# Kernel optimization log

Hardware: AMD Instinct MI355X
Metric: run time of the kernel (lower is better)

Reference implementation:

```python
import jax, jax.numpy as jnp
import numpy as np

HIDDEN = 512
N_LAYERS = 2
SEQ = 512
BATCH = 64
H2 = HIDDEN * 2  # 1024
D_IN = H2 * (N_LAYERS + 1)  # 3072


def setup_inputs() -> dict:
    key = jax.random.key(0)
    ks = jax.random.split(key, 4)
    state = jax.random.normal(ks[0], (N_LAYERS, BATCH, H2), dtype=jnp.float32)
    encoder_output = jax.random.normal(ks[1], (SEQ, BATCH, H2), dtype=jnp.float32)
    # fc1: xavier_normal with tanh gain (5/3); fc2: kaiming_normal
    xavier_std = (5.0 / 3.0) * np.sqrt(2.0 / (D_IN + H2))
    W1 = jax.random.normal(ks[2], (H2, D_IN), dtype=jnp.float32) * xavier_std
    b1 = jnp.zeros((H2,), dtype=jnp.float32)
    W2 = jax.random.normal(ks[3], (1, H2), dtype=jnp.float32) * np.sqrt(2.0 / H2)
    b2 = jnp.zeros((1,), dtype=jnp.float32)
    return {"state": state, "encoder_output": encoder_output,
            "W1": W1, "b1": b1, "W2": W2, "b2": b2}


def reference(state, encoder_output, W1, b1, W2, b2):
    S, B, h2 = encoder_output.shape
    # (n_layers, B, H2) -> (B, n_layers*H2), broadcast over seq
    st = jnp.transpose(state, (1, 0, 2)).reshape(B, -1)
    st = jnp.broadcast_to(st[:, None, :], (B, S, st.shape[-1]))
    enc = jnp.transpose(encoder_output, (1, 0, 2))  # (B, S, H2)
    concat = jnp.concatenate([st, enc], axis=2)      # (B, S, 3*H2)
    energy = jnp.tanh(jnp.einsum('bsd,hd->bsh', concat, W1) + b1)
    energy = (jnp.einsum('bsh,oh->bso', energy, W2) + b2)  # (B, S, 1)
    energy = jnp.transpose(energy, (0, 2, 1))        # (B, 1, S)
    alpha = jax.nn.softmax(energy, axis=2)           # (B, 1, S)
    context = jnp.einsum('bqs,bsh->qbh', alpha, enc)  # (1, B, H2)
    return context, alpha
```

## Files before the change

### kernel.cpp

```cpp
#include <hip/hip_runtime.h>
#include <hip/hip_bf16.h>
#include <stdint.h>

#define H2      1024
#define SEQ     512
#define BATCH   64
#define M_TOTAL (SEQ * BATCH)

typedef __attribute__((ext_vector_type(8))) short short8;
typedef __attribute__((ext_vector_type(4))) float f32x4;

__device__ __forceinline__ unsigned pack2_bf16(float lo, float hi) {
    union { __hip_bfloat162 h; unsigned u; } v;
    v.h = __float22bfloat162_rn(make_float2(lo, hi));
    return v.u;
}

__device__ __forceinline__ float fast_tanh(float x) {
    float e = __expf(2.0f * x);
    return __fdividef(e - 1.0f, e + 1.0f);
}

__device__ __forceinline__ void gl_lds16(const unsigned short* g, unsigned short* l) {
    __builtin_amdgcn_global_load_lds(
        (const __attribute__((address_space(1))) unsigned int*)g,
        (__attribute__((address_space(3))) unsigned int*)l, 16, 0, 0);
}

__global__ __launch_bounds__(256) void k_prep(const float* __restrict__ W1,
                                              unsigned short* __restrict__ W1e) {
    int i = blockIdx.x * 256 + threadIdx.x;
    int e = i << 2;
    int h = e >> 10, k = e & 1023;
    float4 v = *(const float4*)(W1 + (size_t)h * 3072 + 2048 + k);
    uint2 o;
    o.x = pack2_bf16(v.x, v.y);
    o.y = pack2_bf16(v.z, v.w);
    *(uint2*)(W1e + ((size_t)h << 10) + k) = o;
}

__global__ __launch_bounds__(256) void k_prep_enc(const float* __restrict__ enc,
                                                  unsigned short* __restrict__ encb) {
    size_t i = ((size_t)blockIdx.x * 256 + threadIdx.x) << 3;
    float4 v0 = *(const float4*)(enc + i);
    float4 v1 = *(const float4*)(enc + i + 4);
    uint4 o;
    o.x = pack2_bf16(v0.x, v0.y); o.y = pack2_bf16(v0.z, v0.w);
    o.z = pack2_bf16(v1.x, v1.y); o.w = pack2_bf16(v1.z, v1.w);
    *(uint4*)(encb + i) = o;
}

__global__ __launch_bounds__(256) void k_stateproj(const float* __restrict__ W1,
                                                   const float* __restrict__ state,
                                                   const float* __restrict__ b1,
                                                   float* __restrict__ sp) {
    int lane = threadIdx.x & 63;
    int wave = threadIdx.x >> 6;
    int mT   = blockIdx.x;
    int c    = lane & 15;
    int kq   = (lane >> 4) << 3;
    int h    = mT * 16 + c;
    int b    = wave * 16 + c;
    const float* ap = W1 + (size_t)h * 3072 + kq;
    f32x4 acc = {0.f, 0.f, 0.f, 0.f};
    #pragma unroll 4
    for (int k0 = 0; k0 < 2048; k0 += 32) {
        int k = k0 + kq;
        float4 a0 = *(const float4*)(ap + k0);
        float4 a1 = *(const float4*)(ap + k0 + 4);
        int l = k >> 10, j = k & 1023;
        const float* bp = state + (((size_t)l * 64 + b) << 10) + j;
        float4 b0 = *(const float4*)bp;
        float4 b1v = *(const float4*)(bp + 4);
        union { short8 s; uint4 u; } fa, fb;
        fa.u.x = pack2_bf16(a0.x, a0.y); fa.u.y = pack2_bf16(a0.z, a0.w);
        fa.u.z = pack2_bf16(a1.x, a1.y); fa.u.w = pack2_bf16(a1.z, a1.w);
        fb.u.x = pack2_bf16(b0.x, b0.y); fb.u.y = pack2_bf16(b0.z, b0.w);
        fb.u.z = pack2_bf16(b1v.x, b1v.y); fb.u.w = pack2_bf16(b1v.z, b1v.w);
        acc = __builtin_amdgcn_mfma_f32_16x16x32_bf16(fa.s, fb.s, acc, 0, 0, 0);
    }
    int quad = lane >> 4;
    int bcol = wave * 16 + c;
    #pragma unroll
    for (int i = 0; i < 4; ++i) {
        int hh = mT * 16 + quad * 4 + i;
        sp[((size_t)bcol << 10) + hh] = acc[i] + b1[hh];
    }
}

#define BM 128
#define BN 128
#define BK 32

__global__ __launch_bounds__(256, 2) void k_energy(const unsigned short* __restrict__ encb,
                                                   const unsigned short* __restrict__ W1e,
                                                   const float* __restrict__ sp,
                                                   const float* __restrict__ W2,
                                                   float* __restrict__ logits) {
    __shared__ unsigned short As[BM * BK];
    __shared__ unsigned short Bs[BN * BK];
    int bid = blockIdx.x;
    int c8  = bid & 7;
    int jj  = bid >> 3;
    int mT  = c8 * 32 + (jj >> 3);
    int nT  = jj & 7;
    int m0  = mT * BM, n0 = nT * BN;
    int tid  = threadIdx.x;
    int lane = tid & 63, wave = tid >> 6;
    int wm   = (wave >> 1) << 6;
    int wn   = (wave & 1) << 6;

    int r    = lane >> 2;
    int kk   = (lane & 3) << 3;
    int srow = wave * 32 + r;
    const unsigned short* gA = encb + (size_t)(m0 + srow) * H2 + kk;
    const unsigned short* gB = W1e  + (size_t)(n0 + srow) * H2 + kk;
    unsigned short* lA = As + srow * BK + kk;
    unsigned short* lB = Bs + srow * BK + kk;

    f32x4 acc[4][4];
    #pragma unroll
    for (int mi = 0; mi < 4; ++mi)
        #pragma unroll
        for (int ni = 0; ni < 4; ++ni)
            acc[mi][ni] = (f32x4){0.f, 0.f, 0.f, 0.f};

    int c  = lane & 15;
    int kq = (lane >> 4) << 3;
    const unsigned short* afp = As + (wm + c) * BK + kq;
    const unsigned short* bfp = Bs + (wn + c) * BK + kq;

    for (int k0 = 0; k0 < H2; k0 += BK) {
        __syncthreads();
        gl_lds16(gA + k0,           lA);
        gl_lds16(gA + 16 * H2 + k0, lA + 16 * BK);
        gl_lds16(gB + k0,           lB);
        gl_lds16(gB + 16 * H2 + k0, lB + 16 * BK);
        __syncthreads();
        short8 af[4], bf[4];
        #pragma unroll
        for (int i = 0; i < 4; ++i) {
            af[i] = *(const short8*)(afp + (i << 4) * BK);
            bf[i] = *(const short8*)(bfp + (i << 4) * BK);
        }
        #pragma unroll
        for (int mi = 0; mi < 4; ++mi)
            #pragma unroll
            for (int ni = 0; ni < 4; ++ni)
                acc[mi][ni] = __builtin_amdgcn_mfma_f32_16x16x32_bf16(af[mi], bf[ni], acc[mi][ni], 0, 0, 0);
    }

    int quad = lane >> 4;
    float w2v[4];
    int   hcol[4];
    #pragma unroll
    for (int ni = 0; ni < 4; ++ni) {
        hcol[ni] = n0 + wn + ni * 16 + c;
        w2v[ni]  = W2[hcol[ni]];
    }
    #pragma unroll
    for (int mi = 0; mi < 4; ++mi) {
        #pragma unroll
        for (int i = 0; i < 4; ++i) {
            int m = m0 + wm + mi * 16 + quad * 4 + i;
            int b = m & 63;
            const float* sprow = sp + ((size_t)b << 10);
            float t = 0.f;
            #pragma unroll
            for (int ni = 0; ni < 4; ++ni) {
                float e = acc[mi][ni][i] + sprow[hcol[ni]];
                t = fmaf(fast_tanh(e), w2v[ni], t);
            }
            t += __shfl_xor(t, 1);
            t += __shfl_xor(t, 2);
            t += __shfl_xor(t, 4);
            t += __shfl_xor(t, 8);
            if (c == 0) atomicAdd(logits + (size_t)b * 512 + (m >> 6), t);
        }
    }
}

#define LDT 40
__global__ __launch_bounds__(256, 2) void k_energy_f32(const float* __restrict__ enc,
                                                       const unsigned short* __restrict__ W1e,
                                                       const float* __restrict__ sp,
                                                       const float* __restrict__ W2,
                                                       float* __restrict__ logits) {
    __shared__ unsigned short As[BM * LDT];
    __shared__ unsigned short Bs[BN * LDT];
    int bid = blockIdx.x;
    int c8  = bid & 7;
    int jj  = bid >> 3;
    int mT  = c8 * 32 + (jj >> 3);
    int nT  = jj & 7;
    int tid  = threadIdx.x;
    int lane = tid & 63, wave = tid >> 6;
    int wm   = (wave >> 1) << 6;
    int wn   = (wave & 1) << 6;
    int m0   = mT * BM, n0 = nT * BN;

    int arow = tid >> 1;
    int aseg = (tid & 1) << 4;
    const float*          apg = enc + ((size_t)(m0 + arow) << 10) + aseg;
    const unsigned short* wpg = W1e + ((size_t)(n0 + arow) << 10) + aseg;
    unsigned short* asd = As + arow * LDT + aseg;
    unsigned short* bsd = Bs + arow * LDT + aseg;

    f32x4 acc[4][4];
    #pragma unroll
    for (int mi = 0; mi < 4; ++mi)
        #pragma unroll
        for (int ni = 0; ni < 4; ++ni)
            acc[mi][ni] = (f32x4){0.f, 0.f, 0.f, 0.f};

    int c  = lane & 15;
    int kq = (lane >> 4) << 3;
    const unsigned short* afp = As + (wm + c) * LDT + kq;
    const unsigned short* bfp = Bs + (wn + c) * LDT + kq;

    for (int k0 = 0; k0 < 1024; k0 += BK) {
        float4 a0 = *(const float4*)(apg + k0);
        float4 a1 = *(const float4*)(apg + k0 + 4);
        float4 a2 = *(const float4*)(apg + k0 + 8);
        float4 a3 = *(const float4*)(apg + k0 + 12);
        uint4  w0 = *(const uint4*)(wpg + k0);
        uint4  w1 = *(const uint4*)(wpg + k0 + 8);
        uint4 pa0, pa1;
        pa0.x = pack2_bf16(a0.x, a0.y); pa0.y = pack2_bf16(a0.z, a0.w);
        pa0.z = pack2_bf16(a1.x, a1.y); pa0.w = pack2_bf16(a1.z, a1.w);
        pa1.x = pack2_bf16(a2.x, a2.y); pa1.y = pack2_bf16(a2.z, a2.w);
        pa1.z = pack2_bf16(a3.x, a3.y); pa1.w = pack2_bf16(a3.z, a3.w);
        __syncthreads();
        *(uint4*)asd       = pa0;
        *(uint4*)(asd + 8) = pa1;
        *(uint4*)bsd       = w0;
        *(uint4*)(bsd + 8) = w1;
        __syncthreads();
        short8 af[4], bf[4];
        #pragma unroll
        for (int i = 0; i < 4; ++i) {
            af[i] = *(const short8*)(afp + (i << 4) * LDT);
            bf[i] = *(const short8*)(bfp + (i << 4) * LDT);
        }
        #pragma unroll
        for (int mi = 0; mi < 4; ++mi)
            #pragma unroll
            for (int ni = 0; ni < 4; ++ni)
                acc[mi][ni] = __builtin_amdgcn_mfma_f32_16x16x32_bf16(af[mi], bf[ni], acc[mi][ni], 0, 0, 0);
    }

    int quad = lane >> 4;
    float w2v[4];
    int   hcol[4];
    #pragma unroll
    for (int ni = 0; ni < 4; ++ni) {
        hcol[ni] = n0 + wn + ni * 16 + c;
        w2v[ni]  = W2[hcol[ni]];
    }
    #pragma unroll
    for (int mi = 0; mi < 4; ++mi) {
        #pragma unroll
        for (int i = 0; i < 4; ++i) {
            int m = m0 + wm + mi * 16 + quad * 4 + i;
            int b = m & 63;
            const float* sprow = sp + ((size_t)b << 10);
            float t = 0.f;
            #pragma unroll
            for (int ni = 0; ni < 4; ++ni) {
                float e = acc[mi][ni][i] + sprow[hcol[ni]];
                t = fmaf(fast_tanh(e), w2v[ni], t);
            }
            t += __shfl_xor(t, 1);
            t += __shfl_xor(t, 2);
            t += __shfl_xor(t, 4);
            t += __shfl_xor(t, 8);
            if (c == 0) atomicAdd(logits + (size_t)b * 512 + (m >> 6), t);
        }
    }
}

__global__ __launch_bounds__(256) void k_softmax(const float* __restrict__ logits,
                                                 float* __restrict__ alpha) {
    int b = blockIdx.x;
    int tid = threadIdx.x;
    int lane = tid & 63, wave = tid >> 6;
    float v0 = logits[(size_t)b * 512 + tid];
    float v1 = logits[(size_t)b * 512 + 256 + tid];
    float mx = fmaxf(v0, v1);
    #pragma unroll
    for (int o = 32; o; o >>= 1) mx = fmaxf(mx, __shfl_xor(mx, o));
    __shared__ float redm[4];
    if (lane == 0) redm[wave] = mx;
    __syncthreads();
    mx = fmaxf(fmaxf(redm[0], redm[1]), fmaxf(redm[2], redm[3]));
    float e0 = __expf(v0 - mx), e1 = __expf(v1 - mx);
    float s = e0 + e1;
    #pragma unroll
    for (int o = 32; o; o >>= 1) s += __shfl_xor(s, o);
    __shared__ float reds[4];
    if (lane == 0) reds[wave] = s;
    __syncthreads();
    s = reds[0] + reds[1] + reds[2] + reds[3];
    float inv = 1.0f / s;
    alpha[(size_t)b * 512 + tid]       = e0 * inv;
    alpha[(size_t)b * 512 + 256 + tid] = e1 * inv;
}

__global__ __launch_bounds__(256) void k_context(const float* __restrict__ enc,
                                                 const float* __restrict__ alpha,
                                                 float* __restrict__ ctx) {
    int b  = blockIdx.x & 63;
    int sc = blockIdx.x >> 6;
    int h  = threadIdx.x << 2;
    float4 acc = make_float4(0.f, 0.f, 0.f, 0.f);
    int sbase = sc * 64;
    #pragma unroll 4
    for (int si = 0; si < 64; ++si) {
        int s = sbase + si;
        float a = alpha[(size_t)b * 512 + s];
        float4 e = *(const float4*)(enc + (((size_t)s * 64 + b) << 10) + h);
        acc.x = fmaf(a, e.x, acc.x);
        acc.y = fmaf(a, e.y, acc.y);
        acc.z = fmaf(a, e.z, acc.z);
        acc.w = fmaf(a, e.w, acc.w);
    }
    float* dst = ctx + ((size_t)b << 10) + h;
    atomicAdd(dst + 0, acc.x);
    atomicAdd(dst + 1, acc.y);
    atomicAdd(dst + 2, acc.z);
    atomicAdd(dst + 3, acc.w);
}

extern "C" void kernel_launch(void* const* d_in, const int* in_sizes, int n_in,
                              void* d_out, int out_size, void* d_ws, size_t ws_size,
                              hipStream_t stream) {
    const float* state = (const float*)d_in[0];
    const float* enc   = (const float*)d_in[1];
    const float* W1    = (const float*)d_in[2];
    const float* b1    = (const float*)d_in[3];
    const float* W2    = (const float*)d_in[4];

    float* ctx   = (float*)d_out;
    float* alpha = (float*)d_out + 65536;

    char* ws = (char*)d_ws;
    unsigned short* W1e    = (unsigned short*)(ws);
    float*          sp     = (float*)(ws + 2097152);
    float*          logits = (float*)(ws + 2097152 + 262144);
    unsigned short* encb   = (unsigned short*)(ws + 2097152 + 262144 + 131072);

    const size_t need_full = 2097152 + 262144 + 131072 + (size_t)M_TOTAL * H2 * 2;

    hipMemsetAsync(logits, 0, 64 * 512 * sizeof(float), stream);
    hipMemsetAsync(ctx, 0, 65536 * sizeof(float), stream);
    k_prep<<<1024, 256, 0, stream>>>(W1, W1e);
    k_stateproj<<<64, 256, 0, stream>>>(W1, state, b1, sp);
    if (ws_size >= need_full) {
        k_prep_enc<<<16384, 256, 0, stream>>>(enc, encb);
        k_energy<<<M_TOTAL / BM * (H2 / BN), 256, 0, stream>>>(encb, W1e, sp, W2, logits);
    } else {
        k_energy_f32<<<M_TOTAL / BM * (H2 / BN), 256, 0, stream>>>(enc, W1e, sp, W2, logits);
    }
    k_softmax<<<64, 256, 0, stream>>>(logits, alpha);
    k_context<<<512, 256, 0, stream>>>(enc, alpha, ctx);
}
```

Measured before the change: 419.6 us.

## Fuse setup kernels and memsets, use MFMA-fragment LDS layout in energy GEMM

Merges the W1 conversion, state projection and encoder bf16 conversion into one launch, with the logits zeroing folded into the setup kernel and the ctx zeroing moved into the softmax kernel, which removes two memsets and two launches. It also changes the k_energy LDS staging so that each 16-row group is stored in fragment order. Each lane then reads its MFMA operand from a contiguous lane*8 offset, which avoids bank conflicts from the old row-strided layout. The risk is added branching in the combined setup kernel and a reliance on the zeroing order of ctx before k_context.

```diff
diff --git a/kernel.cpp b/kernel.cpp
--- a/kernel.cpp
+++ b/kernel.cpp
@@ -27,64 +27,66 @@
         (__attribute__((address_space(3))) unsigned int*)l, 16, 0, 0);
 }
 
-__global__ __launch_bounds__(256) void k_prep(const float* __restrict__ W1,
-                                              unsigned short* __restrict__ W1e) {
-    int i = blockIdx.x * 256 + threadIdx.x;
-    int e = i << 2;
-    int h = e >> 10, k = e & 1023;
-    float4 v = *(const float4*)(W1 + (size_t)h * 3072 + 2048 + k);
-    uint2 o;
-    o.x = pack2_bf16(v.x, v.y);
-    o.y = pack2_bf16(v.z, v.w);
-    *(uint2*)(W1e + ((size_t)h << 10) + k) = o;
-}
-
-__global__ __launch_bounds__(256) void k_prep_enc(const float* __restrict__ enc,
-                                                  unsigned short* __restrict__ encb) {
-    size_t i = ((size_t)blockIdx.x * 256 + threadIdx.x) << 3;
-    float4 v0 = *(const float4*)(enc + i);
-    float4 v1 = *(const float4*)(enc + i + 4);
-    uint4 o;
-    o.x = pack2_bf16(v0.x, v0.y); o.y = pack2_bf16(v0.z, v0.w);
-    o.z = pack2_bf16(v1.x, v1.y); o.w = pack2_bf16(v1.z, v1.w);
-    *(uint4*)(encb + i) = o;
-}
-
-__global__ __launch_bounds__(256) void k_stateproj(const float* __restrict__ W1,
-                                                   const float* __restrict__ state,
-                                                   const float* __restrict__ b1,
-                                                   float* __restrict__ sp) {
-    int lane = threadIdx.x & 63;
-    int wave = threadIdx.x >> 6;
-    int mT   = blockIdx.x;
-    int c    = lane & 15;
-    int kq   = (lane >> 4) << 3;
-    int h    = mT * 16 + c;
-    int b    = wave * 16 + c;
-    const float* ap = W1 + (size_t)h * 3072 + kq;
-    f32x4 acc = {0.f, 0.f, 0.f, 0.f};
-    #pragma unroll 4
-    for (int k0 = 0; k0 < 2048; k0 += 32) {
-        int k = k0 + kq;
-        float4 a0 = *(const float4*)(ap + k0);
-        float4 a1 = *(const float4*)(ap + k0 + 4);
-        int l = k >> 10, j = k & 1023;
-        const float* bp = state + (((size_t)l * 64 + b) << 10) + j;
-        float4 b0 = *(const float4*)bp;
-        float4 b1v = *(const float4*)(bp + 4);
-        union { short8 s; uint4 u; } fa, fb;
-        fa.u.x = pack2_bf16(a0.x, a0.y); fa.u.y = pack2_bf16(a0.z, a0.w);
-        fa.u.z = pack2_bf16(a1.x, a1.y); fa.u.w = pack2_bf16(a1.z, a1.w);
-        fb.u.x = pack2_bf16(b0.x, b0.y); fb.u.y = pack2_bf16(b0.z, b0.w);
-        fb.u.z = pack2_bf16(b1v.x, b1v.y); fb.u.w = pack2_bf16(b1v.z, b1v.w);
-        acc = __builtin_amdgcn_mfma_f32_16x16x32_bf16(fa.s, fb.s, acc, 0, 0, 0);
-    }
-    int quad = lane >> 4;
-    int bcol = wave * 16 + c;
-    #pragma unroll
-    for (int i = 0; i < 4; ++i) {
-        int hh = mT * 16 + quad * 4 + i;
-        sp[((size_t)bcol << 10) + hh] = acc[i] + b1[hh];
+__global__ __launch_bounds__(256) void k_setup(const float* __restrict__ W1,
+                                               const float* __restrict__ b1,
+                                               const float* __restrict__ state,
+                                               const float* __restrict__ enc,
+                                               unsigned short* __restrict__ W1e,
+                                               unsigned short* __restrict__ encb,
+                                               float* __restrict__ logits,
+                                               float* __restrict__ sp) {
+    int blk = blockIdx.x, tid = threadIdx.x;
+    if (blk < 1024) {
+        int i = blk * 256 + tid;
+        int e = i << 2;
+        int h = e >> 10, k = e & 1023;
+        float4 v = *(const float4*)(W1 + (size_t)h * 3072 + 2048 + k);
+        uint2 o;
+        o.x = pack2_bf16(v.x, v.y);
+        o.y = pack2_bf16(v.z, v.w);
+        *(uint2*)(W1e + ((size_t)h << 10) + k) = o;
+        if (blk < 128) logits[i] = 0.f;
+    } else if (blk < 1088) {
+        int mT   = blk - 1024;
+        int lane = tid & 63;
+        int wave = tid >> 6;
+        int c    = lane & 15;
+        int kq   = (lane >> 4) << 3;
+        int h    = mT * 16 + c;
+        int b    = wave * 16 + c;
+        const float* ap = W1 + (size_t)h * 3072 + kq;
+        f32x4 acc = {0.f, 0.f, 0.f, 0.f};
+        #pragma unroll 4
+        for (int k0 = 0; k0 < 2048; k0 += 32) {
+            int k = k0 + kq;
+            float4 a0 = *(const float4*)(ap + k0);
+            float4 a1 = *(const float4*)(ap + k0 + 4);
+            int l = k >> 10, j = k & 1023;
+            const float* bp = state + (((size_t)l * 64 + b) << 10) + j;
+            float4 b0 = *(const float4*)bp;
+            float4 b1v = *(const float4*)(bp + 4);
+            union { short8 s; uint4 u; } fa, fb;
+            fa.u.x = pack2_bf16(a0.x, a0.y); fa.u.y = pack2_bf16(a0.z, a0.w);
+            fa.u.z = pack2_bf16(a1.x, a1.y); fa.u.w = pack2_bf16(a1.z, a1.w);
+            fb.u.x = pack2_bf16(b0.x, b0.y); fb.u.y = pack2_bf16(b0.z, b0.w);
+            fb.u.z = pack2_bf16(b1v.x, b1v.y); fb.u.w = pack2_bf16(b1v.z, b1v.w);
+            acc = __builtin_amdgcn_mfma_f32_16x16x32_bf16(fa.s, fb.s, acc, 0, 0, 0);
+        }
+        int quad = lane >> 4;
+        int bcol = wave * 16 + c;
+        #pragma unroll
+        for (int i = 0; i < 4; ++i) {
+            int hh = mT * 16 + quad * 4 + i;
+            sp[((size_t)bcol << 10) + hh] = acc[i] + b1[hh];
+        }
+    } else {
+        size_t i = ((size_t)(blk - 1088) * 256 + tid) << 3;
+        float4 v0 = *(const float4*)(enc + i);
+        float4 v1 = *(const float4*)(enc + i + 4);
+        uint4 o;
+        o.x = pack2_bf16(v0.x, v0.y); o.y = pack2_bf16(v0.z, v0.w);
+        o.z = pack2_bf16(v1.x, v1.y); o.w = pack2_bf16(v1.z, v1.w);
+        *(uint4*)(encb + i) = o;
     }
 }
 
@@ -110,13 +112,17 @@
     int wm   = (wave >> 1) << 6;
     int wn   = (wave & 1) << 6;
 
-    int r    = lane >> 2;
-    int kk   = (lane & 3) << 3;
-    int srow = wave * 32 + r;
-    const unsigned short* gA = encb + (size_t)(m0 + srow) * H2 + kk;
-    const unsigned short* gB = W1e  + (size_t)(n0 + srow) * H2 + kk;
-    unsigned short* lA = As + srow * BK + kk;
-    unsigned short* lB = Bs + srow * BK + kk;
+    int rowl = lane & 15;
+    int q    = lane >> 4;
+    int rg0  = wave * 2, rg1 = wave * 2 + 1;
+    const unsigned short* gA0 = encb + (size_t)(m0 + rg0 * 16 + rowl) * H2 + q * 8;
+    const unsigned short* gA1 = encb + (size_t)(m0 + rg1 * 16 + rowl) * H2 + q * 8;
+    const unsigned short* gB0 = W1e  + (size_t)(n0 + rg0 * 16 + rowl) * H2 + q * 8;
+    const unsigned short* gB1 = W1e  + (size_t)(n0 + rg1 * 16 + rowl) * H2 + q * 8;
+    unsigned short* lA0 = As + rg0 * 512;
+    unsigned short* lA1 = As + rg1 * 512;
+    unsigned short* lB0 = Bs + rg0 * 512;
+    unsigned short* lB1 = Bs + rg1 * 512;
 
     f32x4 acc[4][4];
     #pragma unroll
@@ -125,23 +131,23 @@
         for (int ni = 0; ni < 4; ++ni)
             acc[mi][ni] = (f32x4){0.f, 0.f, 0.f, 0.f};
 
-    int c  = lane & 15;
-    int kq = (lane >> 4) << 3;
-    const unsigned short* afp = As + (wm + c) * BK + kq;
-    const unsigned short* bfp = Bs + (wn + c) * BK + kq;
+    int ablk = wm >> 4;
+    int bblk = wn >> 4;
+    const unsigned short* afb = As + ablk * 512 + lane * 8;
+    const unsigned short* bfb = Bs + bblk * 512 + lane * 8;
 
     for (int k0 = 0; k0 < H2; k0 += BK) {
         __syncthreads();
-        gl_lds16(gA + k0,           lA);
-        gl_lds16(gA + 16 * H2 + k0, lA + 16 * BK);
-        gl_lds16(gB + k0,           lB);
-        gl_lds16(gB + 16 * H2 + k0, lB + 16 * BK);
+        gl_lds16(gA0 + k0, lA0);
+        gl_lds16(gA1 + k0, lA1);
+        gl_lds16(gB0 + k0, lB0);
+        gl_lds16(gB1 + k0, lB1);
         __syncthreads();
         short8 af[4], bf[4];
         #pragma unroll
         for (int i = 0; i < 4; ++i) {
-            af[i] = *(const short8*)(afp + (i << 4) * BK);
-            bf[i] = *(const short8*)(bfp + (i << 4) * BK);
+            af[i] = *(const short8*)(afb + i * 512);
+            bf[i] = *(const short8*)(bfb + i * 512);
         }
         #pragma unroll
         for (int mi = 0; mi < 4; ++mi)
@@ -150,6 +156,7 @@
                 acc[mi][ni] = __builtin_amdgcn_mfma_f32_16x16x32_bf16(af[mi], bf[ni], acc[mi][ni], 0, 0, 0);
     }
 
+    int c    = lane & 15;
     int quad = lane >> 4;
     float w2v[4];
     int   hcol[4];
@@ -218,7 +225,7 @@
     const unsigned short* afp = As + (wm + c) * LDT + kq;
     const unsigned short* bfp = Bs + (wn + c) * LDT + kq;
 
-    for (int k0 = 0; k0 < 1024; k0 += BK) {
+    for (int k0 = 0; k0 < 1024; k0 += 32) {
         float4 a0 = *(const float4*)(apg + k0);
         float4 a1 = *(const float4*)(apg + k0 + 4);
         float4 a2 = *(const float4*)(apg + k0 + 8);
@@ -280,10 +287,14 @@
 }
 
 __global__ __launch_bounds__(256) void k_softmax(const float* __restrict__ logits,
-                                                 float* __restrict__ alpha) {
+                                                 float* __restrict__ alpha,
+                                                 float* __restrict__ ctx) {
     int b = blockIdx.x;
     int tid = threadIdx.x;
     int lane = tid & 63, wave = tid >> 6;
+    #pragma unroll
+    for (int j = 0; j < 4; ++j)
+        ctx[((size_t)b << 10) + j * 256 + tid] = 0.f;
     float v0 = logits[(size_t)b * 512 + tid];
     float v1 = logits[(size_t)b * 512 + 256 + tid];
     float mx = fmaxf(v0, v1);
@@ -350,17 +361,14 @@
     unsigned short* encb   = (unsigned short*)(ws + 2097152 + 262144 + 131072);
 
     const size_t need_full = 2097152 + 262144 + 131072 + (size_t)M_TOTAL * H2 * 2;
-
-    hipMemsetAsync(logits, 0, 64 * 512 * sizeof(float), stream);
-    hipMemsetAsync(ctx, 0, 65536 * sizeof(float), stream);
-    k_prep<<<1024, 256, 0, stream>>>(W1, W1e);
-    k_stateproj<<<64, 256, 0, stream>>>(W1, state, b1, sp);
-    if (ws_size >= need_full) {
-        k_prep_enc<<<16384, 256, 0, stream>>>(enc, encb);
+    bool full = ws_size >= need_full;
+
+    k_setup<<<full ? 17472 : 1088, 256, 0, stream>>>(W1, b1, state, enc, W1e, encb, logits, sp);
+    if (full) {
         k_energy<<<M_TOTAL / BM * (H2 / BN), 256, 0, stream>>>(encb, W1e, sp, W2, logits);
     } else {
         k_energy_f32<<<M_TOTAL / BM * (H2 / BN), 256, 0, stream>>>(enc, W1e, sp, W2, logits);
     }
-    k_softmax<<<64, 256, 0, stream>>>(logits, alpha);
+    k_softmax<<<64, 256, 0, stream>>>(logits, alpha, ctx);
     k_context<<<512, 256, 0, stream>>>(enc, alpha, ctx);
 }
```

After: 441.2 us. +5.1%, slower.
